# Kernel optimization log

Hardware: AMD Instinct MI355X
Metric: run time of the kernel (lower is better)

The kernel has to match this reference:

```python
import jax, jax.numpy as jnp
import numpy as np

N, C_IN, C_OUT, T, V = 128, 64, 64, 128, 25
GROUPS, K = 8, 3
REL = C_IN // 8  # rel_reduction=8, in_channels>16


def setup_inputs() -> dict:
    key = jax.random.key(0)
    ks = jax.random.split(key, 16)
    f = lambda k, sh, s=0.05: (jax.random.normal(k, sh) * s).astype(jnp.float32)
    return {
        "x0": jax.random.normal(ks[0], (N, C_IN, T, V), jnp.float32),
        "DecoupleA": f(ks[1], (K, GROUPS, V, V), 0.2),
        "A": f(ks[2], (K, V, V), 0.2),
        "alpha": jnp.full((1,), 0.5, jnp.float32),
        "w1": f(ks[3], (K, REL, C_IN)), "b1": f(ks[4], (K, REL)),
        "w2": f(ks[5], (K, REL, C_IN)), "b2": f(ks[6], (K, REL)),
        "w3": f(ks[7], (K, C_OUT, C_IN)), "b3": f(ks[8], (K, C_OUT)),
        "w4": f(ks[9], (K, C_OUT, REL)), "b4": f(ks[10], (K, C_OUT)),
        "Linear_weight": f(ks[11], (C_IN, C_OUT * K)),
        "Linear_bias": f(ks[12], (1, C_OUT * K, 1, 1)),
        "bn0_gamma": jnp.ones((C_OUT * K,), jnp.float32),
        "bn0_beta": jnp.zeros((C_OUT * K,), jnp.float32),
        "ens_w": f(ks[13], (C_OUT, 2 * C_OUT)), "ens_b": f(ks[14], (C_OUT,)),
        "bn_gamma": jnp.full((C_OUT,), 1e-6, jnp.float32),
        "bn_beta": jnp.zeros((C_OUT,), jnp.float32),
    }


def _bn(x, gamma, beta, eps=1e-5):
    # training-mode BatchNorm2d over NCHW: stats over (N, T, V)
    mu = x.mean(axis=(0, 2, 3), keepdims=True)
    var = x.var(axis=(0, 2, 3), keepdims=True)
    return (x - mu) * jax.lax.rsqrt(var + eps) * gamma[None, :, None, None] + beta[None, :, None, None]


def _norm_adj(A):
    # torch: D = A.sum(dim=rows) -> column sums; A @ diag(1/(D+1e-3)) scales columns
    d = A.sum(axis=-2)  # [..., V] column sums
    return A * (1.0 / (d + 0.001))[..., None, :]


def reference(x0, DecoupleA, A, alpha, w1, b1, w2, b2, w3, b3, w4, b4,
              Linear_weight, Linear_bias, bn0_gamma, bn0_beta, ens_w, ens_b,
              bn_gamma, bn_beta):
    n, c_in, t, v = x0.shape
    k, g = DecoupleA.shape[0], DecoupleA.shape[1]
    c_out = w3.shape[1]
    # DecoupleA.repeat(1, out_channels//groups, 1, 1) == tile along channel dim
    learn_A = jnp.tile(DecoupleA, (1, c_out // g, 1, 1))  # [K, C_OUT, V, V]
    norm_A = _norm_adj(learn_A)
    # decoupled linear path
    x = jnp.einsum('nctv,cd->ndtv', x0, Linear_weight) + Linear_bias
    x = _bn(x, bn0_gamma, bn0_beta)
    x = x.reshape(n, k, c_out, t, v)
    x = jnp.einsum('nkctv,kcvw->nctw', x, norm_A)  # [n, C_OUT, t, v]
    # CTRGC branches (conv-then-mean over T == mean-then-1x1 since conv is linear)
    xm = x0.mean(axis=2)  # [n, c_in, v]
    y = jnp.zeros((n, c_out, t, v), x0.dtype)
    for i in range(k):
        x1 = jnp.einsum('ncv,rc->nrv', xm, w1[i]) + b1[i][:, None]
        x2 = jnp.einsum('ncv,rc->nrv', xm, w2[i]) + b2[i][:, None]
        diff = jnp.tanh(x1[:, :, :, None] - x2[:, :, None, :])        # [n, rel, u, w]
        att = jnp.einsum('nruw,or->nouw', diff, w4[i]) + b4[i][None, :, None, None]
        att = att * alpha[0] + A[i][None, None]                        # [n, C_OUT, u, w]
        x3 = jnp.einsum('nctv,oc->notv', x0, w3[i]) + b3[i][None, :, None, None]
        y = y + jnp.einsum('ncuv,nctu->nctv', att, x3)
    cat = jnp.concatenate([x, y], axis=1)                              # [n, 2*C_OUT, t, v]
    out = jnp.einsum('nctv,oc->notv', cat, ens_w) + ens_b[None, :, None, None]
    out = _bn(out, bn_gamma, bn_beta)
    out = out + x0  # down is identity since in_channels == out_channels
    return jax.nn.relu(out)
```

## Files before the change

kernel.cpp:

```cpp
#include <hip/hip_runtime.h>
#include <cstddef>
#include <cstring>

typedef _Float16 h8 __attribute__((ext_vector_type(8)));
typedef _Float16 h4v __attribute__((ext_vector_type(4)));
typedef float f4 __attribute__((ext_vector_type(4)));
typedef unsigned int u32;
typedef unsigned short u16;

#define MTOT 409600.0f

#define DO_XM  15360000
#define DO_GP  15564800
#define DO_GR  16613376

#define WS_OB16 0
#define WS_ATT  13631488
#define WS_ATTB 23461888
#define WS_BN2P 23666688
#define WS_PAR  23827456
#define WS_CSN  23828000

#define ATT_H 27262976
#define NAB_H 47595520
#define WA_H  47622144
#define W3_H  47634432
#define EW_H  47646720

#define LDS_DYN 116736

__global__ __launch_bounds__(512) void k_gram(const float* __restrict__ x0,
                                              float* __restrict__ gp) {
  __shared__ _Float16 Xs[64 * 128];
  char* smb = (char*)Xs;
  int bid = blockIdx.x, tid = threadIdx.x;
  int n = bid >> 1, sh = bid & 1;
  int base = sh * 1536;
  int niter = sh ? 13 : 12;
  const float* xb = x0 + (size_t)n * 204800;
  int wid = tid >> 6, lane = tid & 63, l15 = lane & 15, l4 = lane >> 4;
  int ca = (wid & 3) * 16;
  int jb0 = (wid >> 2) * 2;
  f4 acc[2] = {{0.f, 0.f, 0.f, 0.f}, {0.f, 0.f, 0.f, 0.f}};
  int sc = tid >> 3, scol = (tid & 7) * 16;
  int swz = (sc & 7) << 4;
  for (int it = 0; it < niter; ++it) {
    int s0 = base + it * 128;
    __syncthreads();
    const float* src = xb + sc * 3200 + s0 + scol;
#pragma unroll
    for (int j = 0; j < 4; ++j) {
      float4 f = *(const float4*)(src + j * 4);
      h4v hv = {(_Float16)f.x, (_Float16)f.y, (_Float16)f.z, (_Float16)f.w};
      *(h4v*)(smb + sc * 256 + (((scol + j * 4) * 2) ^ swz)) = hv;
    }
    __syncthreads();
#pragma unroll
    for (int kk = 0; kk < 4; ++kk) {
      int kb = kk * 64 + l4 * 16;
      int arow = ca + l15;
      h8 af = *(const h8*)(smb + arow * 256 + (kb ^ ((arow & 7) << 4)));
#pragma unroll
      for (int j = 0; j < 2; ++j) {
        int brow = (jb0 + j) * 16 + l15;
        h8 bf = *(const h8*)(smb + brow * 256 + (kb ^ ((brow & 7) << 4)));
        acc[j] = __builtin_amdgcn_mfma_f32_16x16x32_f16(af, bf, acc[j], 0, 0, 0);
      }
    }
  }
  float* o = gp + (size_t)bid * 4096;
#pragma unroll
  for (int j = 0; j < 2; ++j)
#pragma unroll
    for (int q = 0; q < 4; ++q)
      o[(ca + l4 * 4 + q) * 64 + (jb0 + j) * 16 + l15] = acc[j][q];
}

__global__ __launch_bounds__(256) void k_gred(float* __restrict__ dsc) {
  int bid = blockIdx.x, tid = threadIdx.x;
  if (bid < 16) {
    int idx = bid * 256 + tid;
    const float* gp = dsc + DO_GP;
    float s0 = 0.f, s1 = 0.f, s2 = 0.f, s3 = 0.f;
    for (int b = 0; b < 256; b += 4) {
      s0 += gp[(size_t)b * 4096 + idx];
      s1 += gp[(size_t)(b + 1) * 4096 + idx];
      s2 += gp[(size_t)(b + 2) * 4096 + idx];
      s3 += gp[(size_t)(b + 3) * 4096 + idx];
    }
    dsc[DO_GR + idx] = (s0 + s1) + (s2 + s3);
  } else {
    __shared__ float red[64][5];
    int c = tid >> 2, j = tid & 3;
    float s = 0.f;
    for (int nn = j; nn < 128; nn += 4) {
      const float* xmp = dsc + DO_XM + (size_t)(nn * 64 + c) * 25;
      for (int v = 0; v < 25; ++v) s += xmp[v];
    }
    red[c][j] = s;
    __syncthreads();
    if (j == 0)
      dsc[DO_GR + 4096 + c] = 128.f * (red[c][0] + red[c][1] + red[c][2] + red[c][3]);
  }
}

__global__ __launch_bounds__(256) void k_xm(const float* __restrict__ x0,
                                            float* __restrict__ dsc,
                                            float* __restrict__ ws) {
  __shared__ float red[8][32];
  int bid = blockIdx.x;
  int gid = bid * 256 + threadIdx.x;
  if (gid < 204800) ws[WS_ATTB + gid] = 0.f;
  int n = bid >> 6, c = bid & 63;
  int tid = threadIdx.x;
  int tq = tid >> 5, v = tid & 31;
  const float* xb = x0 + (size_t)(n * 64 + c) * 3200;
  float s = 0.f;
  if (v < 25) {
    for (int j = 0; j < 16; j++) s += xb[(tq + 8 * j) * 25 + v];
  }
  red[tq][v] = s;
  __syncthreads();
  if (tq == 0 && v < 25) {
    float tot = 0.f;
#pragma unroll
    for (int q = 0; q < 8; q++) tot += red[q][v];
    dsc[DO_XM + (size_t)(n * 64 + c) * 25 + v] = tot * (1.0f / 128.0f);
  }
}

__global__ __launch_bounds__(256) void k_prep(const float* __restrict__ DA,
                                              const float* __restrict__ w3,
                                              const float* __restrict__ ensw,
                                              float* __restrict__ wsF) {
  int bid = blockIdx.x, tid = threadIdx.x;
  _Float16* wsH = (_Float16*)wsF;
  if (bid < 3) {
    if (tid < 200) {
      int k = bid, g = tid / 25, w = tid % 25;
      const float* base = DA + (k * 8 + g) * 625 + w;
      float s = 0.f;
      for (int v = 0; v < 25; v++) s += base[v * 25];
      float inv = 1.0f / (s + 0.001f);
      wsF[WS_CSN + k * 200 + g * 25 + w] = s * inv;
      _Float16* dst = wsH + NAB_H + (size_t)((k * 8 + g) * 32 + w) * 32;
      for (int v = 0; v < 25; v++) dst[v] = (_Float16)(base[v * 25] * inv);
      for (int v = 25; v < 32; v++) dst[v] = (_Float16)0.f;
    }
  } else if (bid == 3) {
    for (int idx = tid; idx < 5376; idx += 256) {
      int kg = idx / 224, r = idx % 224;
      int w = 25 + r / 32, v = r & 31;
      wsH[NAB_H + (size_t)(kg * 32 + w) * 32 + v] = (_Float16)0.f;
    }
  } else if (bid < 12) {
    int i0 = (bid - 4) * 1536;
    for (int i = tid; i < 1536; i += 256)
      wsH[W3_H + i0 + i] = (_Float16)w3[i0 + i];
  } else {
    int i0 = (bid - 12) * 2048;
    for (int i = tid; i < 2048; i += 256)
      wsH[EW_H + i0 + i] = (_Float16)ensw[i0 + i];
  }
}

__global__ __launch_bounds__(256) void k_bnstat(const float* __restrict__ dsc,
                                                const float* __restrict__ Lw,
                                                const float* __restrict__ g0,
                                                const float* __restrict__ b0,
                                                float* __restrict__ wsF) {
  __shared__ float Gsh[64 * 66];
  __shared__ float Ly[64][17];
  __shared__ float part[16][17];
  __shared__ float a1L[16];
  int bid = blockIdx.x, tid = threadIdx.x;
  int d0 = bid * 16, dl = tid >> 4, r = tid & 15, d = d0 + dl;
  for (int idx = tid; idx < 4096; idx += 256)
    Gsh[(idx >> 6) * 66 + (idx & 63)] = dsc[DO_GR + idx];
  for (int idx = tid; idx < 1024; idx += 256)
    Ly[idx >> 4][idx & 15] = Lw[(idx >> 4) * 192 + d0 + (idx & 15)];
  __syncthreads();
  float acc = 0.f;
#pragma unroll
  for (int cc = 0; cc < 4; ++cc) {
    int c = r * 4 + cc;
    float h = 0.f;
    for (int c2 = 0; c2 < 64; ++c2) h += Gsh[c * 66 + c2] * Ly[c2][dl];
    acc += Ly[c][dl] * h;
  }
  part[dl][r] = acc;
  __syncthreads();
  if (r == 0) {
    float ex2 = 0.f;
#pragma unroll
    for (int i = 0; i < 16; ++i) ex2 += part[dl][i];
    ex2 *= (1.0f / MTOT);
    float mu = 0.f;
    for (int c = 0; c < 64; ++c) mu += dsc[DO_GR + 4096 + c] * Ly[c][dl];
    mu *= (1.0f / MTOT);
    float var = ex2 - mu * mu;
    float a1 = g0[d] * rsqrtf(var + 1e-5f);
    float b1c = b0[d] - a1 * mu;
    wsF[WS_PAR + 128 + d] = a1;
    wsF[WS_PAR + 320 + d] = b1c;
    a1L[dl] = a1;
  }
  __syncthreads();
  _Float16* wsH = (_Float16*)wsF;
  int k = d >> 6, cg = d & 63;
  float a1v = a1L[dl];
#pragma unroll
  for (int j = 0; j < 4; ++j) {
    int e = r * 4 + j;
    wsH[WA_H + k * 4096 + cg * 64 + e] = (_Float16)(a1v * Lw[e * 192 + d]);
  }
}

__global__ __launch_bounds__(256) void k_att(const float* __restrict__ dsc,
    const float* __restrict__ w1, const float* __restrict__ b1,
    const float* __restrict__ w2, const float* __restrict__ b2,
    const float* __restrict__ w4, const float* __restrict__ b4,
    const float* __restrict__ Ag, const float* __restrict__ alpha,
    const float* __restrict__ b3, float* __restrict__ wsF) {
  __shared__ float xms[1600];
  __shared__ float x1s[200];
  __shared__ float x2s[200];
  __shared__ float Td[5000];
  int bid = blockIdx.x, tid = threadIdx.x;
  int n = bid / 3, i = bid % 3;
  for (int idx = tid; idx < 1600; idx += 256)
    xms[idx] = dsc[DO_XM + (size_t)n * 1600 + idx];
  __syncthreads();
  for (int idx = tid; idx < 400; idx += 256) {
    int r = (idx % 200) / 25, u = idx % 25;
    const float* wv = (idx < 200 ? w1 : w2) + (i * 8 + r) * 64;
    float acc = (idx < 200 ? b1 : b2)[i * 8 + r];
    for (int c = 0; c < 64; c++) acc += xms[c * 25 + u] * wv[c];
    if (idx < 200) x1s[r * 25 + u] = acc; else x2s[r * 25 + u] = acc;
  }
  __syncthreads();
  for (int idx = tid; idx < 5000; idx += 256) {
    int r = idx / 625, u = (idx % 625) / 25, w = idx % 25;
    Td[idx] = tanhf(x1s[r * 25 + u] - x2s[r * 25 + w]);
  }
  __syncthreads();
  float al = alpha[0];
  u32* attW = (u32*)wsF;
  for (int p = tid; p < 1600; p += 256) {
    int o = p / 25, w = p % 25;
    float w4r[8];
#pragma unroll
    for (int r = 0; r < 8; r++) w4r[r] = w4[(i * 64 + o) * 8 + r];
    float b4v = b4[i * 64 + o];
    const float* AgW = Ag + i * 625 + w;
    float asum = 0.f;
    size_t rowH = (size_t)ATT_H + ((size_t)((n * 3 + i) * 64 + o) * 25 + w) * 32;
    u32* row = attW + rowH / 2;
    for (int up = 0; up < 16; ++up) {
      u32 word = 0;
#pragma unroll
      for (int h = 0; h < 2; ++h) {
        int u = up * 2 + h;
        float v = 0.f;
        if (u < 25) {
          float acc = b4v;
#pragma unroll
          for (int r = 0; r < 8; r++) acc += w4r[r] * Td[r * 625 + u * 25 + w];
          v = al * acc + AgW[u * 25];
          asum += v;
        }
        union { _Float16 hf; u16 b; } cv;
        cv.hf = (_Float16)v;
        word |= ((u32)cv.b) << (16 * h);
      }
      row[up] = word;
    }
    atomicAdd(&wsF[WS_ATTB + (size_t)n * 1600 + p], b3[i * 64 + o] * asum);
  }
}

__device__ __forceinline__ void stageX(const float* __restrict__ xn, char* sm, int tid) {
  for (int u = tid; u < 6400; u += 1024) {
    int cg = u / 400, s = u - cg * 400;
    int c0 = cg * 4;
    const float* p = xn + c0 * 3200 + s;
    float a = p[0], b = p[3200], c = p[6400], d = p[9600];
    h4v hv = {(_Float16)a, (_Float16)b, (_Float16)c, (_Float16)d};
    *(h4v*)(sm + s * 128 + ((c0 * 2) ^ ((s & 7) << 4))) = hv;
  }
}
__device__ __forceinline__ void zeroHpads(char* sm, int tid) {
  for (int idx = tid; idx < 7168; idx += 1024) {
    int c = idx / 112, r = idx % 112;
    int t = r / 7, u = 25 + r % 7;
    int hs = (((t & 3) ^ ((c >> 2) & 3)) << 4);
    *(_Float16*)(sm + 51200 + c * 1024 + t * 64 + ((u * 2) ^ hs)) = (_Float16)0.f;
  }
}
__device__ __forceinline__ void gemm64(const _Float16* __restrict__ Aw, char* sm,
                                       int mt, int nt0, int nt1, int lane) {
  int l15 = lane & 15, l4 = lane >> 4;
  h8 a0 = *(const h8*)(Aw + (mt * 16 + l15) * 64 + l4 * 8);
  h8 a1 = *(const h8*)(Aw + (mt * 16 + l15) * 64 + 32 + l4 * 8);
  int s = nt0 * 16 + l15;
  int t = s / 25, u = s - t * 25;
  int hsc = ((mt * 4 + l4) & 3) << 4;
  for (int nt = nt0; nt < nt1; ++nt) {
    int sw = (s & 7) << 4;
    const char* rb = sm + s * 128;
    h8 b0 = *(const h8*)(rb + ((l4 * 16) ^ sw));
    h8 b1 = *(const h8*)(rb + ((64 + l4 * 16) ^ sw));
    f4 acc = {0.f, 0.f, 0.f, 0.f};
    acc = __builtin_amdgcn_mfma_f32_16x16x32_f16(a0, b0, acc, 0, 0, 0);
    acc = __builtin_amdgcn_mfma_f32_16x16x32_f16(a1, b1, acc, 0, 0, 0);
    int hs = ((t & 3) << 4) ^ hsc;
    char* wb = sm + 51200 + (mt * 16 + l4 * 4) * 1024 + t * 64 + ((u * 2) ^ hs);
#pragma unroll
    for (int q = 0; q < 4; ++q)
      *(_Float16*)(wb + q * 1024) = (_Float16)acc[q];
    s += 16;
    u += 16;
    if (u >= 25) { u -= 25; ++t; }
  }
}

__global__ __launch_bounds__(1024, 4) void kAB(const float* __restrict__ x0,
                                               float* ws,
                                               const float* __restrict__ ensb) {
  extern __shared__ char sm[];
  __shared__ float redS[128];
  __shared__ float attBs[1600];
  __shared__ float cbS[1600];
  const _Float16* wsH = (const _Float16*)ws;
  int tid = threadIdx.x, bid = blockIdx.x;
  int lb = (bid & 7) * 128 + (bid >> 3);
  int n = lb >> 3, tile = lb & 7;
  int wid = tid >> 6, lane = tid & 63, l15 = lane & 15, l4 = lane >> 4;
  int mt = wid & 3, q4 = wid >> 2, g = wid & 7;
  int nt0 = q4 ? 1 + 6 * q4 : 0;
  int nt1 = q4 ? nt0 + 6 : 7;
  if (tid < 128) redS[tid] = 0.f;
  for (int idx = tid; idx < 1600; idx += 1024)
    attBs[idx] = ws[WS_ATTB + (size_t)n * 1600 + idx];
  for (int idx = tid; idx < 1600; idx += 1024) {
    int c = idx / 25, w = idx - c * 25;
    int gg = c & 7;
    float s = 0.f;
#pragma unroll
    for (int k = 0; k < 3; ++k)
      s += ws[WS_PAR + 320 + k * 64 + c] * ws[WS_CSN + k * 200 + gg * 25 + w];
    cbS[idx] = s;
  }
  stageX(x0 + (size_t)n * 204800 + tile * 400, sm, tid);
  zeroHpads(sm, tid);
  __syncthreads();
  f4 accx[4][2], accy[4][2];
#pragma unroll
  for (int a = 0; a < 4; a++)
#pragma unroll
    for (int b = 0; b < 2; b++) {
      accx[a][b] = (f4){0.f, 0.f, 0.f, 0.f};
      accy[a][b] = (f4){0.f, 0.f, 0.f, 0.f};
    }
  for (int k = 0; k < 3; ++k) {
    gemm64(wsH + WA_H + k * 4096, sm, mt, nt0, nt1, lane);
    __syncthreads();
#pragma unroll
    for (int mt2 = 0; mt2 < 4; ++mt2) {
      int c = mt2 * 16 + wid;
      int hs = (((l15 & 3) ^ ((c >> 2) & 3)) << 4);
      h8 aH = *(const h8*)(sm + 51200 + c * 1024 + l15 * 64 + ((l4 * 16) ^ hs));
#pragma unroll
      for (int nt2 = 0; nt2 < 2; ++nt2) {
        const _Float16* nb = wsH + NAB_H +
            (size_t)((k * 8 + g) * 32 + nt2 * 16 + l15) * 32 + l4 * 8;
        accx[mt2][nt2] = __builtin_amdgcn_mfma_f32_16x16x32_f16(
            aH, *(const h8*)nb, accx[mt2][nt2], 0, 0, 0);
      }
    }
    __syncthreads();
  }
  for (int i = 0; i < 3; ++i) {
    gemm64(wsH + W3_H + i * 4096, sm, mt, nt0, nt1, lane);
    __syncthreads();
#pragma unroll
    for (int mt2 = 0; mt2 < 4; ++mt2) {
      int c = mt2 * 16 + wid;
      int hs = (((l15 & 3) ^ ((c >> 2) & 3)) << 4);
      h8 aX = *(const h8*)(sm + 51200 + c * 1024 + l15 * 64 + ((l4 * 16) ^ hs));
#pragma unroll
      for (int nt2 = 0; nt2 < 2; ++nt2) {
        int v = nt2 * 16 + l15;
        int vc = v < 25 ? v : 0;
        const _Float16* ab = wsH + ATT_H +
            ((size_t)((n * 3 + i) * 64 + c) * 25 + vc) * 32 + l4 * 8;
        accy[mt2][nt2] = __builtin_amdgcn_mfma_f32_16x16x32_f16(
            aX, *(const h8*)ab, accy[mt2][nt2], 0, 0, 0);
      }
    }
    __syncthreads();
  }
#pragma unroll
  for (int mt2 = 0; mt2 < 4; ++mt2) {
    int c = mt2 * 16 + wid;
#pragma unroll
    for (int nt2 = 0; nt2 < 2; ++nt2) {
      int w = nt2 * 16 + l15;
      if (w < 25) {
        float cbv = cbS[c * 25 + w];
        float abv = attBs[c * 25 + w];
#pragma unroll
        for (int q = 0; q < 4; ++q) {
          int t = l4 * 4 + q;
          int s = t * 25 + w;
          int sw = (s & 7) << 4;
          *(_Float16*)(sm + s * 256 + ((c * 2) ^ sw)) =
              (_Float16)(accx[mt2][nt2][q] + cbv);
          *(_Float16*)(sm + s * 256 + (((64 + c) * 2) ^ sw)) =
              (_Float16)(accy[mt2][nt2][q] + abv);
        }
      }
    }
  }
  __syncthreads();
  h8 ea[4];
#pragma unroll
  for (int ks = 0; ks < 4; ++ks)
    ea[ks] = *(const h8*)(wsH + EW_H + (mt * 16 + l15) * 128 + ks * 32 + l4 * 8);
  float eb[4];
#pragma unroll
  for (int q = 0; q < 4; ++q) eb[q] = ensb[mt * 16 + l4 * 4 + q];
  float lsum[4] = {0.f, 0.f, 0.f, 0.f}, lss[4] = {0.f, 0.f, 0.f, 0.f};
  u16* ob16 = (u16*)ws;
  for (int nt = nt0; nt < nt1; ++nt) {
    int s = nt * 16 + l15;
    int sw = (s & 7) << 4;
    f4 acc = {0.f, 0.f, 0.f, 0.f};
#pragma unroll
    for (int ks = 0; ks < 4; ++ks) {
      h8 b = *(const h8*)(sm + s * 256 + (((ks * 32 + l4 * 8) * 2) ^ sw));
      acc = __builtin_amdgcn_mfma_f32_16x16x32_f16(ea[ks], b, acc, 0, 0, 0);
    }
    size_t ob = (size_t)n * 204800 + (size_t)tile * 400 + s;
#pragma unroll
    for (int q = 0; q < 4; ++q) {
      int o = mt * 16 + l4 * 4 + q;
      union { _Float16 hf; u16 b; } cv;
      cv.hf = (_Float16)(acc[q] + eb[q]);
      ob16[ob + (size_t)o * 3200] = cv.b;
      float val = (float)cv.hf;
      lsum[q] += val;
      lss[q] += val * val;
    }
  }
#pragma unroll
  for (int q = 0; q < 4; ++q) {
#pragma unroll
    for (int d = 1; d < 16; d <<= 1) {
      lsum[q] += __shfl_xor(lsum[q], d);
      lss[q] += __shfl_xor(lss[q], d);
    }
  }
  if (l15 == 0) {
#pragma unroll
    for (int q = 0; q < 4; ++q) {
      int o = mt * 16 + l4 * 4 + q;
      atomicAdd(&redS[o], lsum[q]);
      atomicAdd(&redS[64 + o], lss[q]);
    }
  }
  __syncthreads();
  if (tid < 64) {
    ws[WS_BN2P + (size_t)bid * 128 + tid * 2] = redS[tid];
    ws[WS_BN2P + (size_t)bid * 128 + tid * 2 + 1] = redS[64 + tid];
  }
}

__global__ __launch_bounds__(256) void k_bn2(const float* __restrict__ g2,
                                             const float* __restrict__ b2,
                                             float* __restrict__ ws) {
  __shared__ float rs[256], rss[256];
  int o = blockIdx.x, tid = threadIdx.x;
  float s = 0.f, ss = 0.f;
  for (int b = tid; b < 1024; b += 256) {
    s += ws[WS_BN2P + (size_t)b * 128 + o * 2];
    ss += ws[WS_BN2P + (size_t)b * 128 + o * 2 + 1];
  }
  rs[tid] = s; rss[tid] = ss;
  __syncthreads();
  for (int st = 128; st > 0; st >>= 1) {
    if (tid < st) { rs[tid] += rs[tid + st]; rss[tid] += rss[tid + st]; }
    __syncthreads();
  }
  if (tid == 0) {
    float mu = rs[0] / MTOT;
    float var = rss[0] / MTOT - mu * mu;
    float a2 = g2[o] * rsqrtf(var + 1e-5f);
    ws[WS_PAR + o] = a2;
    ws[WS_PAR + 64 + o] = b2[o] - a2 * mu;
  }
}

__global__ __launch_bounds__(256) void k_final(const float* __restrict__ x0,
                                               const float* __restrict__ ws,
                                               float* __restrict__ dout) {
  size_t g = (size_t)blockIdx.x * 256 + threadIdx.x;
  h4v p = reinterpret_cast<const h4v*>(ws)[g];
  float4 x = reinterpret_cast<const float4*>(x0)[g];
  int o = (int)((g * 4 / 3200) & 63);
  float a2 = ws[WS_PAR + o], bc = ws[WS_PAR + 64 + o];
  float4 r;
  r.x = fmaxf(fmaf(a2, (float)p[0], bc) + x.x, 0.f);
  r.y = fmaxf(fmaf(a2, (float)p[1], bc) + x.y, 0.f);
  r.z = fmaxf(fmaf(a2, (float)p[2], bc) + x.z, 0.f);
  r.w = fmaxf(fmaf(a2, (float)p[3], bc) + x.w, 0.f);
  reinterpret_cast<float4*>(dout)[g] = r;
}

extern "C" void kernel_launch(void* const* d_in, const int* in_sizes, int n_in,
                              void* d_out, int out_size, void* d_ws, size_t ws_size,
                              hipStream_t stream) {
  const float* x0    = (const float*)d_in[0];
  const float* DA    = (const float*)d_in[1];
  const float* Ag    = (const float*)d_in[2];
  const float* alpha = (const float*)d_in[3];
  const float* w1    = (const float*)d_in[4];
  const float* b1    = (const float*)d_in[5];
  const float* w2    = (const float*)d_in[6];
  const float* b2    = (const float*)d_in[7];
  const float* w3    = (const float*)d_in[8];
  const float* b3    = (const float*)d_in[9];
  const float* w4    = (const float*)d_in[10];
  const float* b4    = (const float*)d_in[11];
  const float* Lw    = (const float*)d_in[12];
  const float* g0    = (const float*)d_in[14];
  const float* b0    = (const float*)d_in[15];
  const float* ensw  = (const float*)d_in[16];
  const float* ensb  = (const float*)d_in[17];
  const float* g2    = (const float*)d_in[18];
  const float* b2n   = (const float*)d_in[19];
  float* out = (float*)d_out;
  float* ws  = (float*)d_ws;

  hipFuncSetAttribute((const void*)kAB, hipFuncAttributeMaxDynamicSharedMemorySize, LDS_DYN);

  k_xm<<<8192, 256, 0, stream>>>(x0, out, ws);
  k_gram<<<256, 512, 0, stream>>>(x0, out + DO_GP);
  k_prep<<<16, 256, 0, stream>>>(DA, w3, ensw, ws);
  k_att<<<384, 256, 0, stream>>>(out, w1, b1, w2, b2, w4, b4, Ag, alpha, b3, ws);
  k_gred<<<17, 256, 0, stream>>>(out);
  k_bnstat<<<12, 256, 0, stream>>>(out, Lw, g0, b0, ws);
  kAB<<<1024, 1024, LDS_DYN, stream>>>(x0, ws, ensb);
  k_bn2<<<64, 256, 0, stream>>>(g2, b2n, ws);
  k_final<<<25600, 256, 0, stream>>>(x0, ws, out);
}
```

Baseline: 299.0 us.

## Fuse temporal mean into gram kernel via MFMA selector and prefetch loads

Removes the separate k_xm kernel, which made a full extra pass over x0. The per-vertex temporal mean is now computed inside k_gram as an extra MFMA against a one-hot selector matrix whose entries equal 1/128 in fp16, and results are accumulated with atomics. The gram loop also prefetches the next tile into registers so global loads overlap the MFMA work. Zeroing of the two buffers moves to hipMemsetAsync. The mean is now built from fp16-converted inputs, which slightly lowers its precision, and the atomics make summation order nondeterministic.

```diff
diff --git a/kernel.cpp b/kernel.cpp
--- a/kernel.cpp
+++ b/kernel.cpp
@@ -30,7 +30,7 @@
 #define LDS_DYN 116736
 
 __global__ __launch_bounds__(512) void k_gram(const float* __restrict__ x0,
-                                              float* __restrict__ gp) {
+                                              float* __restrict__ dsc) {
   __shared__ _Float16 Xs[64 * 128];
   char* smb = (char*)Xs;
   int bid = blockIdx.x, tid = threadIdx.x;
@@ -42,19 +42,41 @@
   int ca = (wid & 3) * 16;
   int jb0 = (wid >> 2) * 2;
   f4 acc[2] = {{0.f, 0.f, 0.f, 0.f}, {0.f, 0.f, 0.f, 0.f}};
+  f4 accxm = {0.f, 0.f, 0.f, 0.f};
+  int xm_v = l15 + (wid >> 2) * 16;
   int sc = tid >> 3, scol = (tid & 7) * 16;
   int swz = (sc & 7) << 4;
+  int mmod = (base + l4 * 8) % 25;
+  float4 pf0, pf1, pf2, pf3;
+  {
+    const float* src = xb + sc * 3200 + base + scol;
+    pf0 = *(const float4*)(src);
+    pf1 = *(const float4*)(src + 4);
+    pf2 = *(const float4*)(src + 8);
+    pf3 = *(const float4*)(src + 12);
+  }
   for (int it = 0; it < niter; ++it) {
-    int s0 = base + it * 128;
-    __syncthreads();
-    const float* src = xb + sc * 3200 + s0 + scol;
-#pragma unroll
-    for (int j = 0; j < 4; ++j) {
-      float4 f = *(const float4*)(src + j * 4);
-      h4v hv = {(_Float16)f.x, (_Float16)f.y, (_Float16)f.z, (_Float16)f.w};
-      *(h4v*)(smb + sc * 256 + (((scol + j * 4) * 2) ^ swz)) = hv;
-    }
-    __syncthreads();
+    __syncthreads();
+    {
+      h4v hv;
+      hv = (h4v){(_Float16)pf0.x, (_Float16)pf0.y, (_Float16)pf0.z, (_Float16)pf0.w};
+      *(h4v*)(smb + sc * 256 + (((scol + 0) * 2) ^ swz)) = hv;
+      hv = (h4v){(_Float16)pf1.x, (_Float16)pf1.y, (_Float16)pf1.z, (_Float16)pf1.w};
+      *(h4v*)(smb + sc * 256 + (((scol + 4) * 2) ^ swz)) = hv;
+      hv = (h4v){(_Float16)pf2.x, (_Float16)pf2.y, (_Float16)pf2.z, (_Float16)pf2.w};
+      *(h4v*)(smb + sc * 256 + (((scol + 8) * 2) ^ swz)) = hv;
+      hv = (h4v){(_Float16)pf3.x, (_Float16)pf3.y, (_Float16)pf3.z, (_Float16)pf3.w};
+      *(h4v*)(smb + sc * 256 + (((scol + 12) * 2) ^ swz)) = hv;
+    }
+    __syncthreads();
+    if (it + 1 < niter) {
+      const float* src = xb + sc * 3200 + base + (it + 1) * 128 + scol;
+      pf0 = *(const float4*)(src);
+      pf1 = *(const float4*)(src + 4);
+      pf2 = *(const float4*)(src + 8);
+      pf3 = *(const float4*)(src + 12);
+    }
+    int cm = mmod;
 #pragma unroll
     for (int kk = 0; kk < 4; ++kk) {
       int kb = kk * 64 + l4 * 16;
@@ -66,14 +88,33 @@
         h8 bf = *(const h8*)(smb + brow * 256 + (kb ^ ((brow & 7) << 4)));
         acc[j] = __builtin_amdgcn_mfma_f32_16x16x32_f16(af, bf, acc[j], 0, 0, 0);
       }
-    }
-  }
-  float* o = gp + (size_t)bid * 4096;
+      union { u32 w[4]; h8 v; } bx;
+      int t = cm;
+#pragma unroll
+      for (int p = 0; p < 4; ++p) {
+        int t0 = t >= 25 ? t - 25 : t;
+        int t1 = (t + 1) >= 25 ? t - 24 : t + 1;
+        bx.w[p] = (t0 == xm_v ? 0x2000u : 0u) | (t1 == xm_v ? 0x20000000u : 0u);
+        t += 2;
+      }
+      accxm = __builtin_amdgcn_mfma_f32_16x16x32_f16(af, bx.v, accxm, 0, 0, 0);
+      cm += 7; if (cm >= 25) cm -= 25;
+    }
+    mmod += 3; if (mmod >= 25) mmod -= 25;
+  }
+  float* o = dsc + DO_GP + (size_t)bid * 4096;
 #pragma unroll
   for (int j = 0; j < 2; ++j)
 #pragma unroll
     for (int q = 0; q < 4; ++q)
       o[(ca + l4 * 4 + q) * 64 + (jb0 + j) * 16 + l15] = acc[j][q];
+  if (xm_v < 25) {
+#pragma unroll
+    for (int q = 0; q < 4; ++q) {
+      int c = ca + l4 * 4 + q;
+      atomicAdd(&dsc[DO_XM + (size_t)n * 1600 + c * 25 + xm_v], accxm[q]);
+    }
+  }
 }
 
 __global__ __launch_bounds__(256) void k_gred(float* __restrict__ dsc) {
@@ -101,31 +142,6 @@
     __syncthreads();
     if (j == 0)
       dsc[DO_GR + 4096 + c] = 128.f * (red[c][0] + red[c][1] + red[c][2] + red[c][3]);
-  }
-}
-
-__global__ __launch_bounds__(256) void k_xm(const float* __restrict__ x0,
-                                            float* __restrict__ dsc,
-                                            float* __restrict__ ws) {
-  __shared__ float red[8][32];
-  int bid = blockIdx.x;
-  int gid = bid * 256 + threadIdx.x;
-  if (gid < 204800) ws[WS_ATTB + gid] = 0.f;
-  int n = bid >> 6, c = bid & 63;
-  int tid = threadIdx.x;
-  int tq = tid >> 5, v = tid & 31;
-  const float* xb = x0 + (size_t)(n * 64 + c) * 3200;
-  float s = 0.f;
-  if (v < 25) {
-    for (int j = 0; j < 16; j++) s += xb[(tq + 8 * j) * 25 + v];
-  }
-  red[tq][v] = s;
-  __syncthreads();
-  if (tq == 0 && v < 25) {
-    float tot = 0.f;
-#pragma unroll
-    for (int q = 0; q < 8; q++) tot += red[q][v];
-    dsc[DO_XM + (size_t)(n * 64 + c) * 25 + v] = tot * (1.0f / 128.0f);
   }
 }
 
@@ -544,8 +560,9 @@
 
   hipFuncSetAttribute((const void*)kAB, hipFuncAttributeMaxDynamicSharedMemorySize, LDS_DYN);
 
-  k_xm<<<8192, 256, 0, stream>>>(x0, out, ws);
-  k_gram<<<256, 512, 0, stream>>>(x0, out + DO_GP);
+  hipMemsetAsync(ws + WS_ATTB, 0, 204800 * sizeof(float), stream);
+  hipMemsetAsync(out + DO_XM, 0, 204800 * sizeof(float), stream);
+  k_gram<<<256, 512, 0, stream>>>(x0, out);
   k_prep<<<16, 256, 0, stream>>>(DA, w3, ensw, ws);
   k_att<<<384, 256, 0, stream>>>(out, w1, b1, w2, b2, w4, b4, Ag, alpha, b3, ws);
   k_gred<<<17, 256, 0, stream>>>(out);
```

After: 298.1 us (median of 2 runs). About the same (-0.3%).
